# Kernel tuning notes

Measured on AMD Instinct MI355X. Metric: run time of the kernel, lower is better.

## Reference

```python
import jax, jax.numpy as jnp
import numpy as np

B, S, H, E, TOPK = 8, 512, 1024, 8, 2


def setup_inputs() -> dict:
    key = jax.random.key(0)
    ks = jax.random.split(key, 10)
    D = 2 * H
    inp = {
        "vector": jax.random.normal(ks[0], (B, S, D), dtype=jnp.float32),
        # gate weights (Linear(H, E)): stored as [H, E] for x @ W + b
        "Wg": jax.random.normal(ks[1], (H, E), dtype=jnp.float32) * 0.02,
        "bg": jnp.zeros((E,), dtype=jnp.float32),
        "Wf": jax.random.normal(ks[2], (H, E), dtype=jnp.float32) * 0.02,
        "bf": jnp.zeros((E,), dtype=jnp.float32),
        # expert MLP weights, stacked over experts: Linear(2H,2H) -> ReLU -> Linear(2H,2H)
        "W1": jax.random.normal(ks[3], (E, D, D), dtype=jnp.float32) * 0.02,
        "b1": jnp.zeros((E, D), dtype=jnp.float32),
        "W2": jax.random.normal(ks[4], (E, D, D), dtype=jnp.float32) * 0.02,
        "b2": jnp.zeros((E, D), dtype=jnp.float32),
        # combine weights (config['initializer_weight'])
        "weight": jnp.ones((2,), dtype=jnp.float32),
        "top_k": TOPK,
    }
    return inp


def reference(vector, Wg, bg, Wf, bf, W1, b1, W2, b2, weight, top_k):
    h = Wg.shape[0]
    n_exp = Wg.shape[1]
    # gate_g on first half, softmax, then top-k sparsify (scatter of topk values)
    rout_g = jax.nn.softmax(vector[:, :, :h] @ Wg + bg, axis=-1)           # [B,S,E]
    vals, idx = jax.lax.top_k(rout_g, top_k)                               # [B,S,k]
    route_g = jnp.sum(jax.nn.one_hot(idx, n_exp, dtype=vals.dtype) * vals[..., None], axis=-2)  # [B,S,E]
    # gate_f on second half: dense softmax routing
    rout_f = jax.nn.softmax(vector[:, :, h:2 * h] @ Wf + bf, axis=-1)      # [B,S,E]
    # dense expert computation for every token (dropout = identity at eval)
    hidden = jax.nn.relu(jnp.einsum('bsd,edh->bseh', vector, W1) + b1)     # [B,S,E,2H]
    expert_out = jnp.einsum('bseh,ehd->bsed', hidden, W2) + b2             # [B,S,E,2H]
    out0 = weight[0] * jnp.einsum('bsed,bse->bsd', expert_out[..., :h], route_g)
    out1 = weight[1] * jnp.einsum('bsed,bse->bsd', expert_out[..., h:2 * h], rout_f)
    return (out0, out1)
```

## Files before the change

### kernel.cpp

```cpp
#include <hip/hip_runtime.h>

#define TOKENS 4096
#define DDIM   2048
#define HDIM   1024
#define NEXP   8
#define GK     2048
#define GN     2048

typedef __bf16 bf16_t;
typedef __bf16 bf16x8 __attribute__((ext_vector_type(8)));
typedef __bf16 bf16x4 __attribute__((ext_vector_type(4)));
typedef float  f32x4  __attribute__((ext_vector_type(4)));

__device__ inline void gld_lds16(const bf16_t* g, bf16_t* l) {
  __builtin_amdgcn_global_load_lds(
      (const __attribute__((address_space(1))) void*)g,
      (__attribute__((address_space(3))) void*)l, 16, 0, 0);
}

__global__ __launch_bounds__(256)
void k_routing(const float* __restrict__ vec,
               const float* __restrict__ Wg, const float* __restrict__ bg,
               const float* __restrict__ Wf, const float* __restrict__ bfv,
               const float* __restrict__ wgt,
               float* __restrict__ c0, float* __restrict__ c1)
{
  const int wave = threadIdx.x >> 6;
  const int lane = threadIdx.x & 63;
  const int m = blockIdx.x * 4 + wave;
  const float* v = vec + (size_t)m * DDIM;

  float ag[NEXP], af[NEXP];
#pragma unroll
  for (int e = 0; e < NEXP; ++e) { ag[e] = 0.f; af[e] = 0.f; }

  for (int i = lane; i < HDIM; i += 64) {
    const float xg = v[i];
    const float xf = v[HDIM + i];
    const float4 wg0 = *(const float4*)(Wg + i * NEXP);
    const float4 wg1 = *(const float4*)(Wg + i * NEXP + 4);
    const float4 wf0 = *(const float4*)(Wf + i * NEXP);
    const float4 wf1 = *(const float4*)(Wf + i * NEXP + 4);
    ag[0] += xg * wg0.x; ag[1] += xg * wg0.y; ag[2] += xg * wg0.z; ag[3] += xg * wg0.w;
    ag[4] += xg * wg1.x; ag[5] += xg * wg1.y; ag[6] += xg * wg1.z; ag[7] += xg * wg1.w;
    af[0] += xf * wf0.x; af[1] += xf * wf0.y; af[2] += xf * wf0.z; af[3] += xf * wf0.w;
    af[4] += xf * wf1.x; af[5] += xf * wf1.y; af[6] += xf * wf1.z; af[7] += xf * wf1.w;
  }
#pragma unroll
  for (int e = 0; e < NEXP; ++e) {
#pragma unroll
    for (int off = 32; off >= 1; off >>= 1) {
      ag[e] += __shfl_xor(ag[e], off, 64);
      af[e] += __shfl_xor(af[e], off, 64);
    }
  }
  if (lane == 0) {
    float g[NEXP], f[NEXP];
    float mg = -1e30f, mf = -1e30f;
#pragma unroll
    for (int e = 0; e < NEXP; ++e) {
      g[e] = ag[e] + bg[e]; mg = fmaxf(mg, g[e]);
      f[e] = af[e] + bfv[e]; mf = fmaxf(mf, f[e]);
    }
    float sg = 0.f, sf = 0.f;
#pragma unroll
    for (int e = 0; e < NEXP; ++e) {
      g[e] = expf(g[e] - mg); sg += g[e];
      f[e] = expf(f[e] - mf); sf += f[e];
    }
    const float rg = 1.f / sg, rf = 1.f / sf;
#pragma unroll
    for (int e = 0; e < NEXP; ++e) { g[e] *= rg; f[e] *= rf; }
    int i1 = 0;
#pragma unroll
    for (int e = 1; e < NEXP; ++e) if (g[e] > g[i1]) i1 = e;
    int i2 = (i1 == 0) ? 1 : 0;
#pragma unroll
    for (int e = 0; e < NEXP; ++e) if (e != i1 && g[e] > g[i2]) i2 = e;
    const float w0 = wgt[0], w1 = wgt[1];
#pragma unroll
    for (int e = 0; e < NEXP; ++e) {
      c0[e * TOKENS + m] = (e == i1 || e == i2) ? w0 * g[e] : 0.f;
      c1[e * TOKENS + m] = w1 * f[e];
    }
  }
}

__global__ __launch_bounds__(256)
void k_cvt(const float* __restrict__ in, bf16_t* __restrict__ out)
{
  const size_t i = ((size_t)blockIdx.x * 256 + threadIdx.x) * 8;
  const float4 a = *(const float4*)(in + i);
  const float4 b = *(const float4*)(in + i + 4);
  bf16x8 o;
  o[0] = (bf16_t)a.x; o[1] = (bf16_t)a.y; o[2] = (bf16_t)a.z; o[3] = (bf16_t)a.w;
  o[4] = (bf16_t)b.x; o[5] = (bf16_t)b.y; o[6] = (bf16_t)b.z; o[7] = (bf16_t)b.w;
  *(bf16x8*)(out + i) = o;
}

#define TP 68
__global__ __launch_bounds__(256)
void k_cvt_wt(const float* __restrict__ W, bf16_t* __restrict__ Wt)
{
  __shared__ __attribute__((aligned(16))) bf16_t tile[64 * TP];
  const size_t eoff = (size_t)blockIdx.z * DDIM * DDIM;
  const float* w = W + eoff;
  bf16_t* wt = Wt + eoff;
  const int k0 = blockIdx.x * 64;
  const int n0 = blockIdx.y * 64;
  const int t = threadIdx.x;
  const int c4 = (t & 15) * 4;
  const int rb = (t >> 4) * 4;
#pragma unroll
  for (int rr = 0; rr < 4; ++rr) {
    const int r = rb + rr;
    const float4 v = *(const float4*)(w + (size_t)(k0 + r) * DDIM + n0 + c4);
    tile[(c4 + 0) * TP + r] = (bf16_t)v.x;
    tile[(c4 + 1) * TP + r] = (bf16_t)v.y;
    tile[(c4 + 2) * TP + r] = (bf16_t)v.z;
    tile[(c4 + 3) * TP + r] = (bf16_t)v.w;
  }
  __syncthreads();
  const int nl = t >> 2;
  const int kq = (t & 3) * 16;
  bf16_t* dst = wt + (size_t)(n0 + nl) * DDIM + k0 + kq;
#pragma unroll
  for (int j2 = 0; j2 < 4; ++j2) {
    bf16x4 u = *(const bf16x4*)(&tile[nl * TP + kq + j2 * 4]);
    *(bf16x4*)(dst + j2 * 4) = u;
  }
}

__global__ __launch_bounds__(256, 2)
void k_gemm_relu(const bf16_t* __restrict__ A, const bf16_t* __restrict__ W1t,
                 const float* __restrict__ b1, bf16_t* __restrict__ Hd)
{
  __shared__ __attribute__((aligned(16))) bf16_t As[128 * 32];
  __shared__ __attribute__((aligned(16))) bf16_t Bs[128 * 32];
  const int e = blockIdx.z;
  const bf16_t* Bt = W1t + (size_t)e * GK * GN;
  const float* bias = b1 + (size_t)e * GN;
  bf16_t* H = Hd + (size_t)e * TOKENS * GN;

  const int t = threadIdx.x;
  const int wave = t >> 6;
  const int lane = t & 63;
  const int m0 = blockIdx.x * 128;
  const int n0 = blockIdx.y * 128;
  const int wm = (wave >> 1) << 6;
  const int wn = (wave & 1) << 6;

  f32x4 acc[4][4] = {};

  const bf16_t* aP0 = A + (size_t)(m0 + (t >> 2)) * GK + (t & 3) * 8;
  const bf16_t* aP1 = aP0 + (size_t)64 * GK;
  const bf16_t* bP0 = Bt + (size_t)(n0 + (t >> 2)) * GK + (t & 3) * 8;
  const bf16_t* bP1 = bP0 + (size_t)64 * GK;
  bf16_t* lA0 = As + wave * 512;
  bf16_t* lA1 = As + 2048 + wave * 512;
  bf16_t* lB0 = Bs + wave * 512;
  bf16_t* lB1 = Bs + 2048 + wave * 512;

  const int fr = lane & 15;
  const int kq = (lane >> 4) * 8;

  for (int k0 = 0; k0 < GK; k0 += 32) {
    gld_lds16(aP0 + k0, lA0);
    gld_lds16(aP1 + k0, lA1);
    gld_lds16(bP0 + k0, lB0);
    gld_lds16(bP1 + k0, lB1);
    __syncthreads();
    bf16x8 afr[4], bfr[4];
#pragma unroll
    for (int i = 0; i < 4; ++i) {
      afr[i] = *(const bf16x8*)(As + (wm + i * 16 + fr) * 32 + kq);
      bfr[i] = *(const bf16x8*)(Bs + (wn + i * 16 + fr) * 32 + kq);
    }
#pragma unroll
    for (int i = 0; i < 4; ++i)
#pragma unroll
      for (int j = 0; j < 4; ++j)
        acc[i][j] = __builtin_amdgcn_mfma_f32_16x16x32_bf16(afr[i], bfr[j], acc[i][j], 0, 0, 0);
    __syncthreads();
  }

  const int col = lane & 15;
  const int rq  = (lane >> 4) * 4;
#pragma unroll
  for (int j = 0; j < 4; ++j) {
    const int gn = n0 + wn + j * 16 + col;
    const float bv = bias[gn];
#pragma unroll
    for (int i = 0; i < 4; ++i) {
      const int gm = m0 + wm + i * 16 + rq;
#pragma unroll
      for (int r = 0; r < 4; ++r) {
        float v = acc[i][j][r] + bv;
        v = v > 0.f ? v : 0.f;
        H[(size_t)(gm + r) * GN + gn] = (bf16_t)v;
      }
    }
  }
}

__global__ __launch_bounds__(256, 2)
void k_gemm2_sum(const bf16_t* __restrict__ Hd, const bf16_t* __restrict__ W2t,
                 const float* __restrict__ b2,
                 const float* __restrict__ c0, const float* __restrict__ c1,
                 float* __restrict__ out0, float* __restrict__ out1)
{
  __shared__ __attribute__((aligned(16))) bf16_t As[128 * 32];
  __shared__ __attribute__((aligned(16))) bf16_t Bs[128 * 32];
  __shared__ float cs[NEXP][128];
  __shared__ float bs[NEXP][128];

  const int t = threadIdx.x;
  const int wave = t >> 6;
  const int lane = t & 63;
  const int m0 = blockIdx.x * 128;
  const int n0 = blockIdx.y * 128;
  const int wm = (wave >> 1) << 6;
  const int wn = (wave & 1) << 6;

  const bool hi = (n0 >= HDIM);
  const float* cc = hi ? c1 : c0;

#pragma unroll
  for (int idx = t; idx < NEXP * 128; idx += 256) {
    const int e = idx >> 7, r = idx & 127;
    cs[e][r] = cc[e * TOKENS + m0 + r];
    bs[e][r] = b2[e * DDIM + n0 + r];
  }

  f32x4 fin[4][4] = {};

  const int fr = lane & 15;
  const int kq = (lane >> 4) * 8;
  const int rowOff = (t >> 2);
  const int kOff = (t & 3) * 8;
  bf16_t* lA0 = As + wave * 512;
  bf16_t* lA1 = As + 2048 + wave * 512;
  bf16_t* lB0 = Bs + wave * 512;
  bf16_t* lB1 = Bs + 2048 + wave * 512;

  for (int e = 0; e < NEXP; ++e) {
    const bf16_t* aP0 = Hd + (size_t)e * TOKENS * GK + (size_t)(m0 + rowOff) * GK + kOff;
    const bf16_t* aP1 = aP0 + (size_t)64 * GK;
    const bf16_t* bP0 = W2t + (size_t)e * GN * GK + (size_t)(n0 + rowOff) * GK + kOff;
    const bf16_t* bP1 = bP0 + (size_t)64 * GK;

    f32x4 acc[4][4] = {};
    for (int k0 = 0; k0 < GK; k0 += 32) {
      gld_lds16(aP0 + k0, lA0);
      gld_lds16(aP1 + k0, lA1);
      gld_lds16(bP0 + k0, lB0);
      gld_lds16(bP1 + k0, lB1);
      __syncthreads();
      bf16x8 afr[4], bfr[4];
#pragma unroll
      for (int i = 0; i < 4; ++i) {
        afr[i] = *(const bf16x8*)(As + (wm + i * 16 + fr) * 32 + kq);
        bfr[i] = *(const bf16x8*)(Bs + (wn + i * 16 + fr) * 32 + kq);
      }
#pragma unroll
      for (int i = 0; i < 4; ++i)
#pragma unroll
        for (int j = 0; j < 4; ++j)
          acc[i][j] = __builtin_amdgcn_mfma_f32_16x16x32_bf16(afr[i], bfr[j], acc[i][j], 0, 0, 0);
      __syncthreads();
    }

    const int colL = wn + (lane & 15);
    const int rqL  = wm + (lane >> 4) * 4;
#pragma unroll
    for (int j = 0; j < 4; ++j) {
      const float bv = bs[e][colL + j * 16];
#pragma unroll
      for (int i = 0; i < 4; ++i) {
#pragma unroll
        for (int r = 0; r < 4; ++r) {
          const float ce = cs[e][rqL + i * 16 + r];
          fin[i][j][r] += ce * (acc[i][j][r] + bv);
        }
      }
    }
  }

  const int col = lane & 15;
  const int rq  = (lane >> 4) * 4;
#pragma unroll
  for (int j = 0; j < 4; ++j) {
    const int gn = n0 + wn + j * 16 + col;
    float* obase = hi ? (out1 + (gn - HDIM)) : (out0 + gn);
#pragma unroll
    for (int i = 0; i < 4; ++i) {
      const int gm = m0 + wm + i * 16 + rq;
#pragma unroll
      for (int r = 0; r < 4; ++r)
        obase[(size_t)(gm + r) * HDIM] = fin[i][j][r];
    }
  }
}

__global__ __launch_bounds__(256, 2)
void k_gemm_out(const bf16_t* __restrict__ A, const bf16_t* __restrict__ Bt,
                const float* __restrict__ bias,
                const float* __restrict__ c0, const float* __restrict__ c1,
                float* __restrict__ out0, float* __restrict__ out1, const int accum)
{
  __shared__ __attribute__((aligned(16))) bf16_t As[128 * 32];
  __shared__ __attribute__((aligned(16))) bf16_t Bs[128 * 32];
  const int t = threadIdx.x;
  const int wave = t >> 6;
  const int lane = t & 63;
  const int m0 = blockIdx.x * 128;
  const int n0 = blockIdx.y * 128;
  const int wm = (wave >> 1) << 6;
  const int wn = (wave & 1) << 6;

  f32x4 acc[4][4] = {};

  const bf16_t* aP0 = A + (size_t)(m0 + (t >> 2)) * GK + (t & 3) * 8;
  const bf16_t* aP1 = aP0 + (size_t)64 * GK;
  const bf16_t* bP0 = Bt + (size_t)(n0 + (t >> 2)) * GK + (t & 3) * 8;
  const bf16_t* bP1 = bP0 + (size_t)64 * GK;
  bf16_t* lA0 = As + wave * 512;
  bf16_t* lA1 = As + 2048 + wave * 512;
  bf16_t* lB0 = Bs + wave * 512;
  bf16_t* lB1 = Bs + 2048 + wave * 512;

  const int fr = lane & 15;
  const int kq = (lane >> 4) * 8;

  for (int k0 = 0; k0 < GK; k0 += 32) {
    gld_lds16(aP0 + k0, lA0);
    gld_lds16(aP1 + k0, lA1);
    gld_lds16(bP0 + k0, lB0);
    gld_lds16(bP1 + k0, lB1);
    __syncthreads();
    bf16x8 afr[4], bfr[4];
#pragma unroll
    for (int i = 0; i < 4; ++i) {
      afr[i] = *(const bf16x8*)(As + (wm + i * 16 + fr) * 32 + kq);
      bfr[i] = *(const bf16x8*)(Bs + (wn + i * 16 + fr) * 32 + kq);
    }
#pragma unroll
    for (int i = 0; i < 4; ++i)
#pragma unroll
      for (int j = 0; j < 4; ++j)
        acc[i][j] = __builtin_amdgcn_mfma_f32_16x16x32_bf16(afr[i], bfr[j], acc[i][j], 0, 0, 0);
    __syncthreads();
  }

  const int col = lane & 15;
  const int rq  = (lane >> 4) * 4;
#pragma unroll
  for (int j = 0; j < 4; ++j) {
    const int gn = n0 + wn + j * 16 + col;
    const float bv = bias[gn];
    const bool lo = gn < HDIM;
    float* obase = lo ? (out0 + gn) : (out1 + (gn - HDIM));
    const float* cc = lo ? c0 : c1;
#pragma unroll
    for (int i = 0; i < 4; ++i) {
      const int gmB = m0 + wm + i * 16 + rq;
#pragma unroll
      for (int r = 0; r < 4; ++r) {
        const int gm = gmB + r;
        float v = (acc[i][j][r] + bv) * cc[gm];
        float* dst = obase + (size_t)gm * HDIM;
        if (accum) v += *dst;
        *dst = v;
      }
    }
  }
}

extern "C" void kernel_launch(void* const* d_in, const int* in_sizes, int n_in,
                              void* d_out, int out_size, void* d_ws, size_t ws_size,
                              hipStream_t stream)
{
  const float* vec = (const float*)d_in[0];
  const float* Wg  = (const float*)d_in[1];
  const float* bg  = (const float*)d_in[2];
  const float* Wf  = (const float*)d_in[3];
  const float* bfv = (const float*)d_in[4];
  const float* W1  = (const float*)d_in[5];
  const float* b1  = (const float*)d_in[6];
  const float* W2  = (const float*)d_in[7];
  const float* b2  = (const float*)d_in[8];
  const float* wgt = (const float*)d_in[9];

  float* out0 = (float*)d_out;
  float* out1 = out0 + (size_t)TOKENS * HDIM;

  char* base = (char*)d_ws;
  const size_t XB = (size_t)TOKENS * DDIM * 2;
  const size_t HB = (size_t)NEXP * TOKENS * DDIM * 2;
  const size_t WT = (size_t)NEXP * DDIM * DDIM * 2;

  bf16_t* Xbf = (bf16_t*)base;
  float*  c0  = (float*)(base + XB);
  float*  c1  = c0 + (size_t)NEXP * TOKENS;
  size_t off = XB + 2 * (size_t)NEXP * TOKENS * 4;

  k_routing<<<dim3(TOKENS / 4), 256, 0, stream>>>(vec, Wg, bg, Wf, bfv, wgt, c0, c1);
  k_cvt<<<dim3((TOKENS * DDIM) / 2048), 256, 0, stream>>>(vec, Xbf);

  if (ws_size >= off + HB + 2 * WT) {
    bf16_t* hidden = (bf16_t*)(base + off);
    bf16_t* W1t    = (bf16_t*)(base + off + HB);
    bf16_t* W2t    = (bf16_t*)(base + off + HB + WT);
    k_cvt_wt<<<dim3(32, 32, NEXP), 256, 0, stream>>>(W1, W1t);
    k_cvt_wt<<<dim3(32, 32, NEXP), 256, 0, stream>>>(W2, W2t);
    k_gemm_relu<<<dim3(32, 16, NEXP), 256, 0, stream>>>(Xbf, W1t, b1, hidden);
    k_gemm2_sum<<<dim3(32, 16), 256, 0, stream>>>(hidden, W2t, b2, c0, c1, out0, out1);
  } else {
    bf16_t* hidden = (bf16_t*)(base + off);
    bf16_t* W1t    = hidden + (size_t)TOKENS * DDIM;
    bf16_t* W2t    = W1t + (size_t)DDIM * DDIM;
    for (int e = 0; e < NEXP; ++e) {
      k_cvt_wt<<<dim3(32, 32, 1), 256, 0, stream>>>(W1 + (size_t)e * DDIM * DDIM, W1t);
      k_cvt_wt<<<dim3(32, 32, 1), 256, 0, stream>>>(W2 + (size_t)e * DDIM * DDIM, W2t);
      k_gemm_relu<<<dim3(32, 16, 1), 256, 0, stream>>>(Xbf, W1t, b1 + (size_t)e * DDIM, hidden);
      k_gemm_out<<<dim3(32, 16), 256, 0, stream>>>(
          hidden, W2t, b2 + (size_t)e * DDIM,
          c0 + (size_t)e * TOKENS, c1 + (size_t)e * TOKENS, out0, out1, e > 0);
    }
  }
}
```

Baseline: 1.071 ms.

## Split second GEMM over experts, fuse routing with input conversion, merge weight casts

```diff
diff --git a/kernel.cpp b/kernel.cpp
--- a/kernel.cpp
+++ b/kernel.cpp
@@ -19,32 +19,47 @@
 }
 
 __global__ __launch_bounds__(256)
-void k_routing(const float* __restrict__ vec,
-               const float* __restrict__ Wg, const float* __restrict__ bg,
-               const float* __restrict__ Wf, const float* __restrict__ bfv,
-               const float* __restrict__ wgt,
-               float* __restrict__ c0, float* __restrict__ c1)
+void k_routing_cvt(const float* __restrict__ vec,
+                   const float* __restrict__ Wg, const float* __restrict__ bg,
+                   const float* __restrict__ Wf, const float* __restrict__ bfv,
+                   const float* __restrict__ wgt,
+                   float* __restrict__ c0, float* __restrict__ c1,
+                   bf16_t* __restrict__ Xbf)
 {
   const int wave = threadIdx.x >> 6;
   const int lane = threadIdx.x & 63;
   const int m = blockIdx.x * 4 + wave;
   const float* v = vec + (size_t)m * DDIM;
+  bf16_t* xo = Xbf + (size_t)m * DDIM;
 
   float ag[NEXP], af[NEXP];
 #pragma unroll
   for (int e = 0; e < NEXP; ++e) { ag[e] = 0.f; af[e] = 0.f; }
 
-  for (int i = lane; i < HDIM; i += 64) {
-    const float xg = v[i];
-    const float xf = v[HDIM + i];
-    const float4 wg0 = *(const float4*)(Wg + i * NEXP);
-    const float4 wg1 = *(const float4*)(Wg + i * NEXP + 4);
-    const float4 wf0 = *(const float4*)(Wf + i * NEXP);
-    const float4 wf1 = *(const float4*)(Wf + i * NEXP + 4);
-    ag[0] += xg * wg0.x; ag[1] += xg * wg0.y; ag[2] += xg * wg0.z; ag[3] += xg * wg0.w;
-    ag[4] += xg * wg1.x; ag[5] += xg * wg1.y; ag[6] += xg * wg1.z; ag[7] += xg * wg1.w;
-    af[0] += xf * wf0.x; af[1] += xf * wf0.y; af[2] += xf * wf0.z; af[3] += xf * wf0.w;
-    af[4] += xf * wf1.x; af[5] += xf * wf1.y; af[6] += xf * wf1.z; af[7] += xf * wf1.w;
+#pragma unroll
+  for (int j = 0; j < 8; ++j) {
+    const int base = j * 256 + lane * 4;
+    const float4 x = *(const float4*)(v + base);
+    bf16x4 o; o[0] = (bf16_t)x.x; o[1] = (bf16_t)x.y; o[2] = (bf16_t)x.z; o[3] = (bf16_t)x.w;
+    *(bf16x4*)(xo + base) = o;
+    const float xs[4] = {x.x, x.y, x.z, x.w};
+    if (j < 4) {
+#pragma unroll
+      for (int tt = 0; tt < 4; ++tt) {
+        const float4 w0 = *(const float4*)(Wg + (base + tt) * NEXP);
+        const float4 w1 = *(const float4*)(Wg + (base + tt) * NEXP + 4);
+        ag[0] += xs[tt] * w0.x; ag[1] += xs[tt] * w0.y; ag[2] += xs[tt] * w0.z; ag[3] += xs[tt] * w0.w;
+        ag[4] += xs[tt] * w1.x; ag[5] += xs[tt] * w1.y; ag[6] += xs[tt] * w1.z; ag[7] += xs[tt] * w1.w;
+      }
+    } else {
+#pragma unroll
+      for (int tt = 0; tt < 4; ++tt) {
+        const float4 w0 = *(const float4*)(Wf + (base - HDIM + tt) * NEXP);
+        const float4 w1 = *(const float4*)(Wf + (base - HDIM + tt) * NEXP + 4);
+        af[0] += xs[tt] * w0.x; af[1] += xs[tt] * w0.y; af[2] += xs[tt] * w0.z; af[3] += xs[tt] * w0.w;
+        af[4] += xs[tt] * w1.x; af[5] += xs[tt] * w1.y; af[6] += xs[tt] * w1.z; af[7] += xs[tt] * w1.w;
+      }
+    }
   }
 #pragma unroll
   for (int e = 0; e < NEXP; ++e) {
@@ -86,26 +101,17 @@
   }
 }
 
-__global__ __launch_bounds__(256)
-void k_cvt(const float* __restrict__ in, bf16_t* __restrict__ out)
-{
-  const size_t i = ((size_t)blockIdx.x * 256 + threadIdx.x) * 8;
-  const float4 a = *(const float4*)(in + i);
-  const float4 b = *(const float4*)(in + i + 4);
-  bf16x8 o;
-  o[0] = (bf16_t)a.x; o[1] = (bf16_t)a.y; o[2] = (bf16_t)a.z; o[3] = (bf16_t)a.w;
-  o[4] = (bf16_t)b.x; o[5] = (bf16_t)b.y; o[6] = (bf16_t)b.z; o[7] = (bf16_t)b.w;
-  *(bf16x8*)(out + i) = o;
-}
-
 #define TP 68
 __global__ __launch_bounds__(256)
-void k_cvt_wt(const float* __restrict__ W, bf16_t* __restrict__ Wt)
+void k_cvt_wt(const float* __restrict__ WA, const float* __restrict__ WB,
+              bf16_t* __restrict__ WAt, bf16_t* __restrict__ WBt, const int perTensor)
 {
   __shared__ __attribute__((aligned(16))) bf16_t tile[64 * TP];
-  const size_t eoff = (size_t)blockIdx.z * DDIM * DDIM;
-  const float* w = W + eoff;
-  bf16_t* wt = Wt + eoff;
+  const int z = blockIdx.z;
+  const int e = z % perTensor;
+  const size_t eoff = (size_t)e * DDIM * DDIM;
+  const float* w = ((z < perTensor) ? WA : WB) + eoff;
+  bf16_t* wt = ((z < perTensor) ? WAt : WBt) + eoff;
   const int k0 = blockIdx.x * 64;
   const int n0 = blockIdx.y * 64;
   const int t = threadIdx.x;
@@ -125,9 +131,9 @@
   const int kq = (t & 3) * 16;
   bf16_t* dst = wt + (size_t)(n0 + nl) * DDIM + k0 + kq;
 #pragma unroll
-  for (int j2 = 0; j2 < 4; ++j2) {
-    bf16x4 u = *(const bf16x4*)(&tile[nl * TP + kq + j2 * 4]);
-    *(bf16x4*)(dst + j2 * 4) = u;
+  for (int j2 = 0; j2 < 2; ++j2) {
+    bf16x8 u = *(const bf16x8*)(&tile[nl * TP + kq + j2 * 8]);
+    *(bf16x8*)(dst + j2 * 8) = u;
   }
 }
 
@@ -203,33 +209,37 @@
   }
 }
 
+#define ESPLIT 2
+#define EPER   (NEXP / ESPLIT)
 __global__ __launch_bounds__(256, 2)
-void k_gemm2_sum(const bf16_t* __restrict__ Hd, const bf16_t* __restrict__ W2t,
-                 const float* __restrict__ b2,
-                 const float* __restrict__ c0, const float* __restrict__ c1,
-                 float* __restrict__ out0, float* __restrict__ out1)
+void k_gemm2_split(const bf16_t* __restrict__ Hd, const bf16_t* __restrict__ W2t,
+                   const float* __restrict__ b2,
+                   const float* __restrict__ c0, const float* __restrict__ c1,
+                   float* __restrict__ P)
 {
   __shared__ __attribute__((aligned(16))) bf16_t As[128 * 32];
   __shared__ __attribute__((aligned(16))) bf16_t Bs[128 * 32];
-  __shared__ float cs[NEXP][128];
-  __shared__ float bs[NEXP][128];
+  __shared__ float cs[EPER][128];
+  __shared__ float bs[EPER][128];
 
   const int t = threadIdx.x;
   const int wave = t >> 6;
   const int lane = t & 63;
   const int m0 = blockIdx.x * 128;
   const int n0 = blockIdx.y * 128;
+  const int ks = blockIdx.z;
   const int wm = (wave >> 1) << 6;
   const int wn = (wave & 1) << 6;
 
   const bool hi = (n0 >= HDIM);
   const float* cc = hi ? c1 : c0;
-
-#pragma unroll
-  for (int idx = t; idx < NEXP * 128; idx += 256) {
+  float* Pp = P + (size_t)ks * TOKENS * DDIM;
+
+#pragma unroll
+  for (int idx = t; idx < EPER * 128; idx += 256) {
     const int e = idx >> 7, r = idx & 127;
-    cs[e][r] = cc[e * TOKENS + m0 + r];
-    bs[e][r] = b2[e * DDIM + n0 + r];
+    cs[e][r] = cc[(ks * EPER + e) * TOKENS + m0 + r];
+    bs[e][r] = b2[(ks * EPER + e) * DDIM + n0 + r];
   }
 
   f32x4 fin[4][4] = {};
@@ -243,7 +253,8 @@
   bf16_t* lB0 = Bs + wave * 512;
   bf16_t* lB1 = Bs + 2048 + wave * 512;
 
-  for (int e = 0; e < NEXP; ++e) {
+  for (int ee = 0; ee < EPER; ++ee) {
+    const int e = ks * EPER + ee;
     const bf16_t* aP0 = Hd + (size_t)e * TOKENS * GK + (size_t)(m0 + rowOff) * GK + kOff;
     const bf16_t* aP1 = aP0 + (size_t)64 * GK;
     const bf16_t* bP0 = W2t + (size_t)e * GN * GK + (size_t)(n0 + rowOff) * GK + kOff;
@@ -274,12 +285,12 @@
     const int rqL  = wm + (lane >> 4) * 4;
 #pragma unroll
     for (int j = 0; j < 4; ++j) {
-      const float bv = bs[e][colL + j * 16];
+      const float bv = bs[ee][colL + j * 16];
 #pragma unroll
       for (int i = 0; i < 4; ++i) {
 #pragma unroll
         for (int r = 0; r < 4; ++r) {
-          const float ce = cs[e][rqL + i * 16 + r];
+          const float ce = cs[ee][rqL + i * 16 + r];
           fin[i][j][r] += ce * (acc[i][j][r] + bv);
         }
       }
@@ -291,7 +302,7 @@
 #pragma unroll
   for (int j = 0; j < 4; ++j) {
     const int gn = n0 + wn + j * 16 + col;
-    float* obase = hi ? (out1 + (gn - HDIM)) : (out0 + gn);
+    float* obase = hi ? (Pp + (size_t)TOKENS * HDIM + (gn - HDIM)) : (Pp + gn);
 #pragma unroll
     for (int i = 0; i < 4; ++i) {
       const int gm = m0 + wm + i * 16 + rq;
@@ -300,6 +311,16 @@
         obase[(size_t)(gm + r) * HDIM] = fin[i][j][r];
     }
   }
+}
+
+__global__ __launch_bounds__(256)
+void k_reduce(const float* __restrict__ P, float* __restrict__ out)
+{
+  const size_t i = ((size_t)blockIdx.x * 256 + threadIdx.x) * 4;
+  const float4 a = *(const float4*)(P + i);
+  const float4 b = *(const float4*)(P + (size_t)TOKENS * DDIM + i);
+  float4 o; o.x = a.x + b.x; o.y = a.y + b.y; o.z = a.z + b.z; o.w = a.w + b.w;
+  *(float4*)(out + i) = o;
 }
 
 __global__ __launch_bounds__(256, 2)
@@ -398,30 +419,31 @@
   const size_t XB = (size_t)TOKENS * DDIM * 2;
   const size_t HB = (size_t)NEXP * TOKENS * DDIM * 2;
   const size_t WT = (size_t)NEXP * DDIM * DDIM * 2;
+  const size_t PB = (size_t)ESPLIT * TOKENS * DDIM * 4;
 
   bf16_t* Xbf = (bf16_t*)base;
   float*  c0  = (float*)(base + XB);
   float*  c1  = c0 + (size_t)NEXP * TOKENS;
   size_t off = XB + 2 * (size_t)NEXP * TOKENS * 4;
 
-  k_routing<<<dim3(TOKENS / 4), 256, 0, stream>>>(vec, Wg, bg, Wf, bfv, wgt, c0, c1);
-  k_cvt<<<dim3((TOKENS * DDIM) / 2048), 256, 0, stream>>>(vec, Xbf);
-
-  if (ws_size >= off + HB + 2 * WT) {
+  k_routing_cvt<<<dim3(TOKENS / 4), 256, 0, stream>>>(vec, Wg, bg, Wf, bfv, wgt, c0, c1, Xbf);
+
+  if (ws_size >= off + HB + 2 * WT + PB) {
     bf16_t* hidden = (bf16_t*)(base + off);
     bf16_t* W1t    = (bf16_t*)(base + off + HB);
     bf16_t* W2t    = (bf16_t*)(base + off + HB + WT);
-    k_cvt_wt<<<dim3(32, 32, NEXP), 256, 0, stream>>>(W1, W1t);
-    k_cvt_wt<<<dim3(32, 32, NEXP), 256, 0, stream>>>(W2, W2t);
+    float*  P      = (float*)(base + off + HB + 2 * WT);
+    k_cvt_wt<<<dim3(32, 32, 2 * NEXP), 256, 0, stream>>>(W1, W2, W1t, W2t, NEXP);
     k_gemm_relu<<<dim3(32, 16, NEXP), 256, 0, stream>>>(Xbf, W1t, b1, hidden);
-    k_gemm2_sum<<<dim3(32, 16), 256, 0, stream>>>(hidden, W2t, b2, c0, c1, out0, out1);
+    k_gemm2_split<<<dim3(32, 16, ESPLIT), 256, 0, stream>>>(hidden, W2t, b2, c0, c1, P);
+    k_reduce<<<dim3((TOKENS * DDIM) / 1024), 256, 0, stream>>>(P, out0);
   } else {
     bf16_t* hidden = (bf16_t*)(base + off);
     bf16_t* W1t    = hidden + (size_t)TOKENS * DDIM;
     bf16_t* W2t    = W1t + (size_t)DDIM * DDIM;
     for (int e = 0; e < NEXP; ++e) {
-      k_cvt_wt<<<dim3(32, 32, 1), 256, 0, stream>>>(W1 + (size_t)e * DDIM * DDIM, W1t);
-      k_cvt_wt<<<dim3(32, 32, 1), 256, 0, stream>>>(W2 + (size_t)e * DDIM * DDIM, W2t);
+      k_cvt_wt<<<dim3(32, 32, 2), 256, 0, stream>>>(
+          W1 + (size_t)e * DDIM * DDIM, W2 + (size_t)e * DDIM * DDIM, W1t, W2t, 1);
       k_gemm_relu<<<dim3(32, 16, 1), 256, 0, stream>>>(Xbf, W1t, b1 + (size_t)e * DDIM, hidden);
       k_gemm_out<<<dim3(32, 16), 256, 0, stream>>>(
           hidden, W2t, b2 + (size_t)e * DDIM,
```

After: 1.138 ms. 1.06x slower.
